# Kernel optimization log

Measured on AMD Instinct MI355X. Metric: run time of the kernel, lower is better.

The kernel has to match this reference:

```python
import jax, jax.numpy as jnp
import numpy as np

H, W, SCALE = 480, 640, 8  # full-res grid and coarse downsample factor (hw0_i/hw0_c)


def _struct_feats(pts, anchor_ids):
    """pts: [N, H*W, 3]; anchor_ids: [N, A] int -> [N, L, 4*A] with L=(H//SCALE)*(W//SCALE)."""
    N = pts.shape[0]
    coarse = pts.reshape(N, H, W, 3)[:, ::SCALE, ::SCALE, :].reshape(N, -1, 3)  # [N, L, 3]
    anchors = jnp.take_along_axis(pts, anchor_ids[:, :, None], axis=1)          # [N, A, 3]
    diff = coarse[:, :, None, :] - anchors[:, None, :, :]                        # [N, L, A, 3]
    dist = jnp.sum(diff * diff, axis=-1, keepdims=True)                          # [N, L, A, 1]
    s = jnp.concatenate([diff, dist], axis=-1)                                   # [N, L, A, 4]
    s = s / jnp.sum(jnp.abs(s), axis=-2, keepdims=True)                          # L1 norm over anchor axis
    s = jnp.swapaxes(s, -1, -2).reshape(N, coarse.shape[1], -1)                  # [N, L, 4A]
    return s


def _mlp(x, W1, b1, W2, b2):
    return jax.nn.relu(x @ W1 + b1) @ W2 + b2


def setup_inputs() -> dict:
    key = jax.random.key(0)
    ks = jax.random.split(key, 10)
    N, L, C, A, P = 4, 4800, 256, 128, H * W
    D = C + 4 * A  # 768
    return {
        "feat0": jax.random.normal(ks[0], (N, L, C), jnp.float32),
        "feat1": jax.random.normal(ks[1], (N, L, C), jnp.float32),
        "pts_3d0": jax.random.normal(ks[2], (N, P, 3), jnp.float32),
        "pts_3d1": jax.random.normal(ks[3], (N, P, 3), jnp.float32),
        "anchor_i_ids": jax.random.randint(ks[4], (N, A), 0, P),
        "anchor_j_ids": jax.random.randint(ks[5], (N, A), 0, P),
        "W1": jax.random.normal(ks[6], (D, D), jnp.float32) * (1.0 / np.sqrt(D)),
        "b1": jnp.zeros((D,), jnp.float32),
        "W2": jax.random.normal(ks[7], (D, C), jnp.float32) * (1.0 / np.sqrt(D)),
        "b2": jnp.zeros((C,), jnp.float32),
    }


def reference(feat0, feat1, pts_3d0, pts_3d1, anchor_i_ids, anchor_j_ids, W1, b1, W2, b2):
    s0 = _struct_feats(pts_3d0, anchor_i_ids)  # [N, L, 4A]
    s1 = _struct_feats(pts_3d1, anchor_j_ids)
    aug0 = _mlp(jnp.concatenate([feat0, s0], axis=-1), W1, b1, W2, b2)  # [N, L, C]
    aug1 = _mlp(jnp.concatenate([feat1, s1], axis=-1), W1, b1, W2, b2)
    return (aug0, aug1)
```

## Files before the change

### kernel.cpp

```cpp
#include <hip/hip_runtime.h>
#include <stdint.h>
#include <stddef.h>

typedef __attribute__((ext_vector_type(8))) short short8;
typedef __attribute__((ext_vector_type(4))) short short4v;
typedef __attribute__((ext_vector_type(4))) float f32x4;

#define GLDS16(gp, lp)                                                        \
    __builtin_amdgcn_global_load_lds(                                         \
        (const __attribute__((address_space(1))) void*)(gp),                  \
        (__attribute__((address_space(3))) void*)(lp), 16, 0, 0)

__device__ __forceinline__ unsigned short f2bf(float f) {
    union { float f; uint32_t u; } v;
    v.f = f;
    uint32_t u = v.u;
    u += 0x7FFFu + ((u >> 16) & 1u);
    return (unsigned short)(u >> 16);
}

__global__ __launch_bounds__(1024) void transpose_to_bf16(
    const float* __restrict__ src, unsigned short* __restrict__ dst, int R, int C)
{
    __shared__ float tile[32][33];
    const int c0 = blockIdx.x * 32, r0 = blockIdx.y * 32;
    const int tx = threadIdx.x, ty = threadIdx.y;
    tile[ty][tx] = src[(size_t)(r0 + ty) * C + (c0 + tx)];
    __syncthreads();
    dst[(size_t)(c0 + ty) * R + (r0 + tx)] = f2bf(tile[tx][ty]);
}

__global__ __launch_bounds__(64) void struct_pack(
    const float* __restrict__ feat0, const float* __restrict__ feat1,
    const float* __restrict__ pts0,  const float* __restrict__ pts1,
    const int* __restrict__ ids0,    const int* __restrict__ ids1,
    unsigned short* __restrict__ xw)
{
    const int m = blockIdx.x;
    const int t = m / 19200;
    const int r = m % 19200;
    const int n = r / 4800;
    const int l = r % 4800;
    const float* feat = t ? feat1 : feat0;
    const float* pts  = (t ? pts1 : pts0) + (size_t)n * (307200 * 3);
    const int*   ids  = (t ? ids1 : ids0) + n * 128;
    const int a = threadIdx.x;

    const int lr = l / 80, lc = l % 80;
    const int p  = (lr * 8) * 640 + lc * 8;
    const float cx = pts[p * 3 + 0], cy = pts[p * 3 + 1], cz = pts[p * 3 + 2];

    const int id0 = ids[a], id1 = ids[a + 64];
    const float d0x = cx - pts[id0 * 3 + 0];
    const float d0y = cy - pts[id0 * 3 + 1];
    const float d0z = cz - pts[id0 * 3 + 2];
    const float d0d = d0x * d0x + d0y * d0y + d0z * d0z;
    const float d1x = cx - pts[id1 * 3 + 0];
    const float d1y = cy - pts[id1 * 3 + 1];
    const float d1z = cz - pts[id1 * 3 + 2];
    const float d1d = d1x * d1x + d1y * d1y + d1z * d1z;

    float p0 = fabsf(d0x) + fabsf(d1x);
    float p1 = fabsf(d0y) + fabsf(d1y);
    float p2 = fabsf(d0z) + fabsf(d1z);
    float p3 = d0d + d1d;
#pragma unroll
    for (int off = 32; off; off >>= 1) {
        p0 += __shfl_xor(p0, off);
        p1 += __shfl_xor(p1, off);
        p2 += __shfl_xor(p2, off);
        p3 += __shfl_xor(p3, off);
    }
    const float i0 = 1.0f / p0, i1 = 1.0f / p1, i2 = 1.0f / p2, i3 = 1.0f / p3;

    unsigned short* xrow = xw + (size_t)m * 768;
    const float* frow = feat + (size_t)(n * 4800 + l) * 256;
    const float4 fv = ((const float4*)frow)[a];
    short4v s4;
    s4.x = (short)f2bf(fv.x); s4.y = (short)f2bf(fv.y);
    s4.z = (short)f2bf(fv.z); s4.w = (short)f2bf(fv.w);
    *(short4v*)(xrow + a * 4) = s4;

    xrow[256 + 0 * 128 + a]      = f2bf(d0x * i0);
    xrow[256 + 0 * 128 + a + 64] = f2bf(d1x * i0);
    xrow[256 + 1 * 128 + a]      = f2bf(d0y * i1);
    xrow[256 + 1 * 128 + a + 64] = f2bf(d1y * i1);
    xrow[256 + 2 * 128 + a]      = f2bf(d0z * i2);
    xrow[256 + 2 * 128 + a + 64] = f2bf(d1z * i2);
    xrow[256 + 3 * 128 + a]      = f2bf(d0d * i3);
    xrow[256 + 3 * 128 + a + 64] = f2bf(d1d * i3);
}

template <bool RELU, bool OUT_BF16>
__global__ __launch_bounds__(512, 2) void gemm_8ph(
    const unsigned short* __restrict__ A,
    const unsigned short* __restrict__ Bt,
    const float* __restrict__ bias,
    void* __restrict__ Cout,
    int K, int N, int ntx, int q8, int r8)
{
    extern __shared__ char lds[];
    const int nt = K >> 6;

    const int bid = blockIdx.x;
    const int xcd = bid & 7, idx = bid >> 3;
    const int w = (xcd < r8 ? xcd * (q8 + 1) : r8 * (q8 + 1) + (xcd - r8) * q8) + idx;
    const int n0 = (w % ntx) * 128;
    const int m0 = (w / ntx) * 256;

    const int tid = threadIdx.x;
    const int lane = tid & 63;
    const int wv = tid >> 6;
    const int wr = wv >> 1;
    const int wc = wv & 1;

    const int slr = lane >> 3;
    const int kc  = (lane & 7) ^ slr;
    const unsigned short* gA = A  + (size_t)(m0 + wv * 8 + slr) * K + kc * 8;
    const unsigned short* gB = Bt + (size_t)(n0 + wv * 8 + slr) * K + kc * 8;
    const int ldsW = wv * 1024;

    auto stageA = [&](int buf, int i, int kt) {
        GLDS16(gA + (size_t)i * 64 * K + kt, lds + buf * 49152 + i * 8192 + ldsW);
    };
    auto stageB = [&](int buf, int j, int kt) {
        GLDS16(gB + (size_t)j * 64 * K + kt, lds + buf * 49152 + 32768 + j * 8192 + ldsW);
    };

    const int rsel = lane & 15;
    const int kbh  = lane >> 4;
    const int ck0 = ((kbh) ^ (rsel & 7)) * 16;
    const int ck1 = ((4 + kbh) ^ (rsel & 7)) * 16;
    const int aRowB = (wr * 64 + rsel) * 128;
    const int bRowB = (wc * 64 + rsel) * 128;

    auto LDA = [&](int buf, int mi, int ks) -> short8 {
        return *(const short8*)(lds + buf * 49152 + aRowB + mi * 2048 + (ks ? ck1 : ck0));
    };
    auto LDB = [&](int buf, int ni, int ks) -> short8 {
        return *(const short8*)(lds + buf * 49152 + 32768 + bRowB + ni * 2048 + (ks ? ck1 : ck0));
    };

    f32x4 acc[4][4] = {};
    short8 aF[4][2], bF[4][2];

    {
        stageA(0, 0, 0); stageA(0, 1, 0); stageA(0, 2, 0); stageA(0, 3, 0);
        stageB(0, 0, 0); stageB(0, 1, 0);
        if (nt > 1) {
            stageA(1, 0, 64); stageA(1, 1, 64); stageA(1, 2, 64); stageA(1, 3, 64);
            stageB(1, 0, 64); stageB(1, 1, 64);
        }
    }
    asm volatile("s_waitcnt vmcnt(6)" ::: "memory");
    __builtin_amdgcn_s_barrier();

    for (int t = 0; t < nt; ++t) {
        const int cb = t % 3;
        const int sb = (t + 2) % 3;
        const int kt2 = (t + 2) << 6;
        const bool st = (t + 2) < nt;

        aF[0][0] = LDA(cb, 0, 0); aF[0][1] = LDA(cb, 0, 1);
        aF[1][0] = LDA(cb, 1, 0); aF[1][1] = LDA(cb, 1, 1);
        bF[0][0] = LDB(cb, 0, 0); bF[0][1] = LDB(cb, 0, 1);
        bF[1][0] = LDB(cb, 1, 0); bF[1][1] = LDB(cb, 1, 1);
        if (st) { stageA(sb, 0, kt2); stageA(sb, 1, kt2); }
        __builtin_amdgcn_s_barrier();
        __builtin_amdgcn_s_setprio(1);
#pragma unroll
        for (int i = 0; i < 2; i++)
#pragma unroll
            for (int j = 0; j < 2; j++)
#pragma unroll
                for (int ks = 0; ks < 2; ks++)
                    acc[i][j] = __builtin_amdgcn_mfma_f32_16x16x32_bf16(aF[i][ks], bF[j][ks], acc[i][j], 0, 0, 0);
        __builtin_amdgcn_s_setprio(0);
        __builtin_amdgcn_s_barrier();

        aF[2][0] = LDA(cb, 2, 0); aF[2][1] = LDA(cb, 2, 1);
        aF[3][0] = LDA(cb, 3, 0); aF[3][1] = LDA(cb, 3, 1);
        if (st) { stageA(sb, 2, kt2); stageA(sb, 3, kt2); }
        __builtin_amdgcn_s_barrier();
        __builtin_amdgcn_s_setprio(1);
#pragma unroll
        for (int i = 2; i < 4; i++)
#pragma unroll
            for (int j = 0; j < 2; j++)
#pragma unroll
                for (int ks = 0; ks < 2; ks++)
                    acc[i][j] = __builtin_amdgcn_mfma_f32_16x16x32_bf16(aF[i][ks], bF[j][ks], acc[i][j], 0, 0, 0);
        __builtin_amdgcn_s_setprio(0);
        __builtin_amdgcn_s_barrier();

        bF[2][0] = LDB(cb, 2, 0); bF[2][1] = LDB(cb, 2, 1);
        bF[3][0] = LDB(cb, 3, 0); bF[3][1] = LDB(cb, 3, 1);
        if (st) { stageB(sb, 0, kt2); }
        __builtin_amdgcn_s_barrier();
        __builtin_amdgcn_s_setprio(1);
#pragma unroll
        for (int i = 0; i < 2; i++)
#pragma unroll
            for (int j = 2; j < 4; j++)
#pragma unroll
                for (int ks = 0; ks < 2; ks++)
                    acc[i][j] = __builtin_amdgcn_mfma_f32_16x16x32_bf16(aF[i][ks], bF[j][ks], acc[i][j], 0, 0, 0);
        __builtin_amdgcn_s_setprio(0);
        __builtin_amdgcn_s_barrier();

        if (st) { stageB(sb, 1, kt2); }
        __builtin_amdgcn_s_barrier();
        __builtin_amdgcn_s_setprio(1);
#pragma unroll
        for (int i = 2; i < 4; i++)
#pragma unroll
            for (int j = 2; j < 4; j++)
#pragma unroll
                for (int ks = 0; ks < 2; ks++)
                    acc[i][j] = __builtin_amdgcn_mfma_f32_16x16x32_bf16(aF[i][ks], bF[j][ks], acc[i][j], 0, 0, 0);
        __builtin_amdgcn_s_setprio(0);

        if (st) { asm volatile("s_waitcnt vmcnt(6)" ::: "memory"); }
        else    { asm volatile("s_waitcnt vmcnt(0)" ::: "memory"); }
        __builtin_amdgcn_s_barrier();
    }

    const int crow = (lane >> 4) * 4;
    const int ccol = lane & 15;
#pragma unroll
    for (int j = 0; j < 4; j++) {
        const int col = n0 + wc * 64 + j * 16 + ccol;
        const float bv = bias[col];
#pragma unroll
        for (int i = 0; i < 4; i++) {
#pragma unroll
            for (int rg = 0; rg < 4; rg++) {
                const int row = m0 + wr * 64 + i * 16 + crow + rg;
                float v = acc[i][j][rg] + bv;
                if (RELU) v = fmaxf(v, 0.0f);
                if (OUT_BF16) {
                    ((unsigned short*)Cout)[(size_t)row * N + col] = f2bf(v);
                } else {
                    ((float*)Cout)[(size_t)row * N + col] = v;
                }
            }
        }
    }
}

extern "C" void kernel_launch(void* const* d_in, const int* in_sizes, int n_in,
                              void* d_out, int out_size, void* d_ws, size_t ws_size,
                              hipStream_t stream) {
    const float* feat0 = (const float*)d_in[0];
    const float* feat1 = (const float*)d_in[1];
    const float* pts0  = (const float*)d_in[2];
    const float* pts1  = (const float*)d_in[3];
    const int*   ids0  = (const int*)d_in[4];
    const int*   ids1  = (const int*)d_in[5];
    const float* W1    = (const float*)d_in[6];
    const float* b1    = (const float*)d_in[7];
    const float* W2    = (const float*)d_in[8];
    const float* b2    = (const float*)d_in[9];
    float* out = (float*)d_out;

    char* ws = (char*)d_ws;
    unsigned short* xw  = (unsigned short*)(ws);
    unsigned short* h   = (unsigned short*)(ws + 58982400);
    unsigned short* w1t = (unsigned short*)(ws + 117964800);
    unsigned short* w2t = (unsigned short*)(ws + 119144448);

    const int LDS_BYTES = 147456;
    (void)hipFuncSetAttribute((const void*)&gemm_8ph<true, true>,
                              hipFuncAttributeMaxDynamicSharedMemorySize, LDS_BYTES);
    (void)hipFuncSetAttribute((const void*)&gemm_8ph<false, false>,
                              hipFuncAttributeMaxDynamicSharedMemorySize, LDS_BYTES);

    dim3 tb(32, 32);
    transpose_to_bf16<<<dim3(768 / 32, 768 / 32), tb, 0, stream>>>(W1, w1t, 768, 768);
    transpose_to_bf16<<<dim3(256 / 32, 768 / 32), tb, 0, stream>>>(W2, w2t, 768, 256);

    struct_pack<<<38400, 64, 0, stream>>>(feat0, feat1, pts0, pts1, ids0, ids1, xw);

    gemm_8ph<true, true><<<900, 512, LDS_BYTES, stream>>>(xw, w1t, b1, (void*)h, 768, 768, 6, 112, 4);
    gemm_8ph<false, false><<<300, 512, LDS_BYTES, stream>>>(h, w2t, b2, (void*)out, 768, 256, 2, 37, 4);
}
```

Before: 129.4 us.

## Template GEMM tiles; use 256x256 tiles with split A/B buffering for first GEMM

Result: faster. 125.8 us (-2.8%).

```diff
diff --git a/kernel.cpp b/kernel.cpp
--- a/kernel.cpp
+++ b/kernel.cpp
@@ -91,152 +91,174 @@
     xrow[256 + 3 * 128 + a + 64] = f2bf(d1d * i3);
 }
 
-template <bool RELU, bool OUT_BF16>
-__global__ __launch_bounds__(512, 2) void gemm_8ph(
+template <int MI, int NJ, int WRN_LOG, bool RELU, bool OUT_BF16>
+__global__ __launch_bounds__(512, 2) void gemm_t(
     const unsigned short* __restrict__ A,
     const unsigned short* __restrict__ Bt,
     const float* __restrict__ bias,
     void* __restrict__ Cout,
     int K, int N, int ntx, int q8, int r8)
 {
+    constexpr int WRN = 1 << WRN_LOG;
+    constexpr int WRM = 8 / WRN;
+    constexpr int BM = WRM * MI * 16;
+    constexpr int BN = WRN * NJ * 16;
+    constexpr int ASLOT = BM * 128;
+    constexpr int BSLOT = BN * 128;
+    constexpr int ALD = BM / 64;
+    constexpr int BLD = BN / 64;
+    static_assert(ALD == 4, "vmcnt immediates assume 4 A-loads/wave/tile");
+
     extern __shared__ char lds[];
     const int nt = K >> 6;
 
     const int bid = blockIdx.x;
     const int xcd = bid & 7, idx = bid >> 3;
     const int w = (xcd < r8 ? xcd * (q8 + 1) : r8 * (q8 + 1) + (xcd - r8) * q8) + idx;
-    const int n0 = (w % ntx) * 128;
-    const int m0 = (w / ntx) * 256;
+    const int n0 = (w % ntx) * BN;
+    const int m0 = (w / ntx) * BM;
 
     const int tid = threadIdx.x;
     const int lane = tid & 63;
     const int wv = tid >> 6;
-    const int wr = wv >> 1;
-    const int wc = wv & 1;
+    const int wr = wv >> WRN_LOG;
+    const int wc = wv & (WRN - 1);
 
     const int slr = lane >> 3;
     const int kc  = (lane & 7) ^ slr;
     const unsigned short* gA = A  + (size_t)(m0 + wv * 8 + slr) * K + kc * 8;
     const unsigned short* gB = Bt + (size_t)(n0 + wv * 8 + slr) * K + kc * 8;
-    const int ldsW = wv * 1024;
-
-    auto stageA = [&](int buf, int i, int kt) {
-        GLDS16(gA + (size_t)i * 64 * K + kt, lds + buf * 49152 + i * 8192 + ldsW);
+
+    auto stA = [&](int slot, int i, int kt) {
+        GLDS16(gA + (size_t)i * 64 * K + kt, lds + slot * ASLOT + (i * 64 + wv * 8) * 128);
     };
-    auto stageB = [&](int buf, int j, int kt) {
-        GLDS16(gB + (size_t)j * 64 * K + kt, lds + buf * 49152 + 32768 + j * 8192 + ldsW);
+    auto stB = [&](int slot, int j, int kt) {
+        GLDS16(gB + (size_t)j * 64 * K + kt, lds + 3 * ASLOT + slot * BSLOT + (j * 64 + wv * 8) * 128);
     };
 
     const int rsel = lane & 15;
     const int kbh  = lane >> 4;
     const int ck0 = ((kbh) ^ (rsel & 7)) * 16;
     const int ck1 = ((4 + kbh) ^ (rsel & 7)) * 16;
-    const int aRowB = (wr * 64 + rsel) * 128;
-    const int bRowB = (wc * 64 + rsel) * 128;
-
-    auto LDA = [&](int buf, int mi, int ks) -> short8 {
-        return *(const short8*)(lds + buf * 49152 + aRowB + mi * 2048 + (ks ? ck1 : ck0));
+    const int aRowB = (wr * (MI * 16) + rsel) * 128;
+    const int bRowB = (wc * (NJ * 16) + rsel) * 128;
+
+    auto LDA = [&](int slot, int mi, int ks) -> short8 {
+        return *(const short8*)(lds + slot * ASLOT + aRowB + mi * 2048 + (ks ? ck1 : ck0));
     };
-    auto LDB = [&](int buf, int ni, int ks) -> short8 {
-        return *(const short8*)(lds + buf * 49152 + 32768 + bRowB + ni * 2048 + (ks ? ck1 : ck0));
+    auto LDB = [&](int slot, int nj, int ks) -> short8 {
+        return *(const short8*)(lds + 3 * ASLOT + slot * BSLOT + bRowB + nj * 2048 + (ks ? ck1 : ck0));
     };
 
-    f32x4 acc[4][4] = {};
-    short8 aF[4][2], bF[4][2];
+    f32x4 acc[MI][NJ] = {};
+    short8 aF[MI / 2], bF[NJ];
 
     {
-        stageA(0, 0, 0); stageA(0, 1, 0); stageA(0, 2, 0); stageA(0, 3, 0);
-        stageB(0, 0, 0); stageB(0, 1, 0);
+#pragma unroll
+        for (int i = 0; i < ALD; ++i) stA(0, i, 0);
+#pragma unroll
+        for (int j = 0; j < BLD; ++j) stB(0, j, 0);
         if (nt > 1) {
-            stageA(1, 0, 64); stageA(1, 1, 64); stageA(1, 2, 64); stageA(1, 3, 64);
-            stageB(1, 0, 64); stageB(1, 1, 64);
-        }
+#pragma unroll
+            for (int i = 0; i < ALD; ++i) stA(1, i, 64);
+            asm volatile("s_waitcnt vmcnt(4)" ::: "memory");
+        } else {
+            asm volatile("s_waitcnt vmcnt(0)" ::: "memory");
+        }
+        __builtin_amdgcn_s_barrier();
     }
-    asm volatile("s_waitcnt vmcnt(6)" ::: "memory");
-    __builtin_amdgcn_s_barrier();
-
+
+    int cb3 = 0;
     for (int t = 0; t < nt; ++t) {
-        const int cb = t % 3;
-        const int sb = (t + 2) % 3;
+        const int cb2 = t & 1;
+        const int sb2 = cb2 ^ 1;
+        int sa3 = cb3 + 2; if (sa3 >= 3) sa3 -= 3;
+        const int kt1 = (t + 1) << 6;
         const int kt2 = (t + 2) << 6;
-        const bool st = (t + 2) < nt;
-
-        aF[0][0] = LDA(cb, 0, 0); aF[0][1] = LDA(cb, 0, 1);
-        aF[1][0] = LDA(cb, 1, 0); aF[1][1] = LDA(cb, 1, 1);
-        bF[0][0] = LDB(cb, 0, 0); bF[0][1] = LDB(cb, 0, 1);
-        bF[1][0] = LDB(cb, 1, 0); bF[1][1] = LDB(cb, 1, 1);
-        if (st) { stageA(sb, 0, kt2); stageA(sb, 1, kt2); }
+        const bool stb = (t + 1) < nt;
+        const bool sta = (t + 2) < nt;
+
+#pragma unroll
+        for (int nj = 0; nj < NJ; ++nj) bF[nj] = LDB(cb2, nj, 0);
+#pragma unroll
+        for (int mi = 0; mi < MI / 2; ++mi) aF[mi] = LDA(cb3, mi, 0);
+        if (stb) {
+#pragma unroll
+            for (int j = 0; j < BLD / 2; ++j) stB(sb2, j, kt1);
+        }
         __builtin_amdgcn_s_barrier();
         __builtin_amdgcn_s_setprio(1);
 #pragma unroll
-        for (int i = 0; i < 2; i++)
-#pragma unroll
-            for (int j = 0; j < 2; j++)
-#pragma unroll
-                for (int ks = 0; ks < 2; ks++)
-                    acc[i][j] = __builtin_amdgcn_mfma_f32_16x16x32_bf16(aF[i][ks], bF[j][ks], acc[i][j], 0, 0, 0);
+        for (int mi = 0; mi < MI / 2; ++mi)
+#pragma unroll
+            for (int nj = 0; nj < NJ; ++nj)
+                acc[mi][nj] = __builtin_amdgcn_mfma_f32_16x16x32_bf16(aF[mi], bF[nj], acc[mi][nj], 0, 0, 0);
         __builtin_amdgcn_s_setprio(0);
         __builtin_amdgcn_s_barrier();
 
-        aF[2][0] = LDA(cb, 2, 0); aF[2][1] = LDA(cb, 2, 1);
-        aF[3][0] = LDA(cb, 3, 0); aF[3][1] = LDA(cb, 3, 1);
-        if (st) { stageA(sb, 2, kt2); stageA(sb, 3, kt2); }
+#pragma unroll
+        for (int mi = 0; mi < MI / 2; ++mi) aF[mi] = LDA(cb3, MI / 2 + mi, 0);
+        if (stb) {
+#pragma unroll
+            for (int j = BLD / 2; j < BLD; ++j) stB(sb2, j, kt1);
+        }
         __builtin_amdgcn_s_barrier();
         __builtin_amdgcn_s_setprio(1);
 #pragma unroll
-        for (int i = 2; i < 4; i++)
-#pragma unroll
-            for (int j = 0; j < 2; j++)
-#pragma unroll
-                for (int ks = 0; ks < 2; ks++)
-                    acc[i][j] = __builtin_amdgcn_mfma_f32_16x16x32_bf16(aF[i][ks], bF[j][ks], acc[i][j], 0, 0, 0);
+        for (int mi = 0; mi < MI / 2; ++mi)
+#pragma unroll
+            for (int nj = 0; nj < NJ; ++nj)
+                acc[MI / 2 + mi][nj] = __builtin_amdgcn_mfma_f32_16x16x32_bf16(aF[mi], bF[nj], acc[MI / 2 + mi][nj], 0, 0, 0);
         __builtin_amdgcn_s_setprio(0);
         __builtin_amdgcn_s_barrier();
 
-        bF[2][0] = LDB(cb, 2, 0); bF[2][1] = LDB(cb, 2, 1);
-        bF[3][0] = LDB(cb, 3, 0); bF[3][1] = LDB(cb, 3, 1);
-        if (st) { stageB(sb, 0, kt2); }
+#pragma unroll
+        for (int nj = 0; nj < NJ; ++nj) bF[nj] = LDB(cb2, nj, 1);
+#pragma unroll
+        for (int mi = 0; mi < MI / 2; ++mi) aF[mi] = LDA(cb3, mi, 1);
+        if (sta) { stA(sa3, 0, kt2); stA(sa3, 1, kt2); }
         __builtin_amdgcn_s_barrier();
         __builtin_amdgcn_s_setprio(1);
 #pragma unroll
-        for (int i = 0; i < 2; i++)
-#pragma unroll
-            for (int j = 2; j < 4; j++)
-#pragma unroll
-                for (int ks = 0; ks < 2; ks++)
-                    acc[i][j] = __builtin_amdgcn_mfma_f32_16x16x32_bf16(aF[i][ks], bF[j][ks], acc[i][j], 0, 0, 0);
+        for (int mi = 0; mi < MI / 2; ++mi)
+#pragma unroll
+            for (int nj = 0; nj < NJ; ++nj)
+                acc[mi][nj] = __builtin_amdgcn_mfma_f32_16x16x32_bf16(aF[mi], bF[nj], acc[mi][nj], 0, 0, 0);
         __builtin_amdgcn_s_setprio(0);
         __builtin_amdgcn_s_barrier();
 
-        if (st) { stageB(sb, 1, kt2); }
+#pragma unroll
+        for (int mi = 0; mi < MI / 2; ++mi) aF[mi] = LDA(cb3, MI / 2 + mi, 1);
+        if (sta) { stA(sa3, 2, kt2); stA(sa3, 3, kt2); }
         __builtin_amdgcn_s_barrier();
         __builtin_amdgcn_s_setprio(1);
 #pragma unroll
-        for (int i = 2; i < 4; i++)
-#pragma unroll
-            for (int j = 2; j < 4; j++)
-#pragma unroll
-                for (int ks = 0; ks < 2; ks++)
-                    acc[i][j] = __builtin_amdgcn_mfma_f32_16x16x32_bf16(aF[i][ks], bF[j][ks], acc[i][j], 0, 0, 0);
+        for (int mi = 0; mi < MI / 2; ++mi)
+#pragma unroll
+            for (int nj = 0; nj < NJ; ++nj)
+                acc[MI / 2 + mi][nj] = __builtin_amdgcn_mfma_f32_16x16x32_bf16(aF[mi], bF[nj], acc[MI / 2 + mi][nj], 0, 0, 0);
         __builtin_amdgcn_s_setprio(0);
 
-        if (st) { asm volatile("s_waitcnt vmcnt(6)" ::: "memory"); }
-        else    { asm volatile("s_waitcnt vmcnt(0)" ::: "memory"); }
-        __builtin_amdgcn_s_barrier();
+        if (t + 1 < nt) {
+            if (t + 2 < nt) asm volatile("s_waitcnt vmcnt(4)" ::: "memory");
+            else            asm volatile("s_waitcnt vmcnt(0)" ::: "memory");
+            __builtin_amdgcn_s_barrier();
+        }
+        cb3 = (cb3 + 1 == 3) ? 0 : cb3 + 1;
     }
 
     const int crow = (lane >> 4) * 4;
     const int ccol = lane & 15;
 #pragma unroll
-    for (int j = 0; j < 4; j++) {
-        const int col = n0 + wc * 64 + j * 16 + ccol;
+    for (int nj = 0; nj < NJ; ++nj) {
+        const int col = n0 + wc * (NJ * 16) + nj * 16 + ccol;
         const float bv = bias[col];
 #pragma unroll
-        for (int i = 0; i < 4; i++) {
-#pragma unroll
-            for (int rg = 0; rg < 4; rg++) {
-                const int row = m0 + wr * 64 + i * 16 + crow + rg;
-                float v = acc[i][j][rg] + bv;
+        for (int mi = 0; mi < MI; ++mi) {
+#pragma unroll
+            for (int rg = 0; rg < 4; ++rg) {
+                const int row = m0 + wr * (MI * 16) + mi * 16 + crow + rg;
+                float v = acc[mi][nj][rg] + bv;
                 if (RELU) v = fmaxf(v, 0.0f);
                 if (OUT_BF16) {
                     ((unsigned short*)Cout)[(size_t)row * N + col] = f2bf(v);
@@ -269,11 +291,12 @@
     unsigned short* w1t = (unsigned short*)(ws + 117964800);
     unsigned short* w2t = (unsigned short*)(ws + 119144448);
 
-    const int LDS_BYTES = 147456;
-    (void)hipFuncSetAttribute((const void*)&gemm_8ph<true, true>,
-                              hipFuncAttributeMaxDynamicSharedMemorySize, LDS_BYTES);
-    (void)hipFuncSetAttribute((const void*)&gemm_8ph<false, false>,
-                              hipFuncAttributeMaxDynamicSharedMemorySize, LDS_BYTES);
+    const int LDS1 = 3 * 32768 + 2 * 32768;
+    const int LDS2 = 3 * 32768 + 2 * 16384;
+    (void)hipFuncSetAttribute((const void*)&gemm_t<8, 4, 2, true, true>,
+                              hipFuncAttributeMaxDynamicSharedMemorySize, LDS1);
+    (void)hipFuncSetAttribute((const void*)&gemm_t<4, 4, 1, false, false>,
+                              hipFuncAttributeMaxDynamicSharedMemorySize, LDS2);
 
     dim3 tb(32, 32);
     transpose_to_bf16<<<dim3(768 / 32, 768 / 32), tb, 0, stream>>>(W1, w1t, 768, 768);
@@ -281,6 +304,6 @@
 
     struct_pack<<<38400, 64, 0, stream>>>(feat0, feat1, pts0, pts1, ids0, ids1, xw);
 
-    gemm_8ph<true, true><<<900, 512, LDS_BYTES, stream>>>(xw, w1t, b1, (void*)h, 768, 768, 6, 112, 4);
-    gemm_8ph<false, false><<<300, 512, LDS_BYTES, stream>>>(h, w2t, b2, (void*)out, 768, 256, 2, 37, 4);
-}
+    gemm_t<8, 4, 2, true, true><<<450, 512, LDS1, stream>>>(xw, w1t, b1, (void*)h, 768, 768, 3, 56, 2);
+    gemm_t<4, 4, 1, false, false><<<300, 512, LDS2, stream>>>(h, w2t, b2, (void*)out, 768, 256, 2, 37, 4);
+}
```
